# Kernel tuning notes

Hardware: AMD Instinct MI355X
Metric: run time of the kernel (lower is better)

Reference implementation:

```python
import jax, jax.numpy as jnp
import numpy as np

EPS = 1e-6
NUM_HEADS = 8
HEAD_DIM = 64
ROPE_BASE = 100.0


def _rope_cos_sin(dim, height, width, base=ROPE_BASE):
    quarter = dim // 4
    inv_freq = 1.0 / (base ** (jnp.arange(quarter, dtype=jnp.float32) / quarter))
    freqs_y = jnp.arange(height, dtype=jnp.float32)[:, None] * inv_freq  # (H, q)
    emb_y = jnp.concatenate([freqs_y, freqs_y], axis=-1)                 # (H, dim//2)
    freqs_x = jnp.arange(width, dtype=jnp.float32)[:, None] * inv_freq
    emb_x = jnp.concatenate([freqs_x, freqs_x], axis=-1)                 # (W, dim//2)
    emb_y_grid = jnp.broadcast_to(emb_y[:, None, :], (height, width, dim // 2))
    emb_x_grid = jnp.broadcast_to(emb_x[None, :, :], (height, width, dim // 2))
    full = jnp.concatenate([emb_y_grid, emb_x_grid], axis=-1).reshape(-1, dim)  # (H*W, dim)
    return jnp.cos(full), jnp.sin(full)


def _rotate_half(x):
    x1, x2 = jnp.split(x, 2, axis=-1)
    return jnp.concatenate([-x2, x1], axis=-1)


def setup_inputs() -> dict:
    key = jax.random.key(0)
    ks = jax.random.split(key, 8)
    B, C, H, W = 16, 512, 32, 32
    t_dim = 512
    inner = NUM_HEADS * HEAD_DIM  # 512
    s = 0.02
    return {
        "x": jax.random.normal(ks[0], (B, C, H, W), dtype=jnp.float32),
        "time_emb": jax.random.normal(ks[1], (B, t_dim), dtype=jnp.float32),
        "tm_w1": jax.random.normal(ks[2], (t_dim, t_dim), dtype=jnp.float32) * s,
        "tm_b1": jnp.zeros((t_dim,), dtype=jnp.float32),
        "tm_w2": jax.random.normal(ks[3], (t_dim, 2 * C), dtype=jnp.float32) * s,
        "tm_b2": jnp.zeros((2 * C,), dtype=jnp.float32),
        "qkv_w": jax.random.normal(ks[4], (C, 3 * inner), dtype=jnp.float32) * s,
        "out_w": jax.random.normal(ks[5], (inner, C), dtype=jnp.float32) * s,
        "out_b": jnp.zeros((C,), dtype=jnp.float32),
    }


def reference(x, time_emb, tm_w1, tm_b1, tm_w2, tm_b2, qkv_w, out_w, out_b):
    B, C, H, W = x.shape
    N = H * W
    h, d = NUM_HEADS, HEAD_DIM

    # AdaCLN: channel-wise layernorm with time-conditioned affine modulation
    u = jnp.mean(x, axis=1, keepdims=True)
    s = jnp.mean((x - u) ** 2, axis=1, keepdims=True)
    x_norm = (x - u) / jnp.sqrt(s + EPS)
    emb = jax.nn.silu(time_emb @ tm_w1 + tm_b1) @ tm_w2 + tm_b2  # (B, 2C)
    gamma, beta = jnp.split(emb, 2, axis=1)
    x_norm = x_norm * (1.0 + gamma[:, :, None, None]) + beta[:, :, None, None]

    # (B, C, H, W) -> (B, N, C)
    tokens = x_norm.transpose(0, 2, 3, 1).reshape(B, N, C)

    qkv = tokens @ qkv_w  # (B, N, 3*inner)
    q, k, v = jnp.split(qkv, 3, axis=-1)
    q = q.reshape(B, N, h, d).transpose(0, 2, 1, 3)  # (B, h, N, d)
    k = k.reshape(B, N, h, d).transpose(0, 2, 1, 3)
    v = v.reshape(B, N, h, d).transpose(0, 2, 1, 3)

    cos, sin = _rope_cos_sin(d, H, W)  # (N, d)
    q = q * cos + _rotate_half(q) * sin
    k = k * cos + _rotate_half(k) * sin

    # SDPA, scale = 1/sqrt(head_dim)
    scale = 1.0 / jnp.sqrt(jnp.asarray(d, dtype=q.dtype))
    scores = jnp.einsum("bhqd,bhkd->bhqk", q, k) * scale
    attn = jax.nn.softmax(scores, axis=-1)
    out = jnp.einsum("bhqk,bhkd->bhqd", attn, v)  # (B, h, N, d)

    out = out.transpose(0, 2, 1, 3).reshape(B, N, h * d)
    out = out @ out_w + out_b  # (B, N, C)
    out = out.reshape(B, H, W, C).transpose(0, 3, 1, 2)
    return x + out
```

## Files before the change

### kernel.cpp

```cpp
#include <hip/hip_runtime.h>
#include <stdint.h>
#include <stddef.h>

#define B_  16
#define C_  512
#define N_  1024
#define NH  8
#define HD  64

typedef __attribute__((ext_vector_type(8))) short bf16x8;
typedef __attribute__((ext_vector_type(4))) float f32x4;
typedef __attribute__((ext_vector_type(2))) __bf16 bf16x2t;
typedef __attribute__((ext_vector_type(2))) unsigned uint2v;

__device__ __forceinline__ float bf2f(short s) {
    unsigned u = ((unsigned)(unsigned short)s) << 16;
    return __builtin_bit_cast(float, u);
}
__device__ __forceinline__ unsigned packcvt(float lo, float hi) {
    bf16x2t v = { (__bf16)lo, (__bf16)hi };
    return __builtin_bit_cast(unsigned, v);
}
__device__ __forceinline__ short f2bf_hw(float f) {
    __bf16 b = (__bf16)f;
    return __builtin_bit_cast(short, b);
}
__device__ __forceinline__ float fexp2(float x) {
#if __has_builtin(__builtin_amdgcn_exp2f)
    return __builtin_amdgcn_exp2f(x);
#else
    return exp2f(x);
#endif
}
__device__ __forceinline__ void plswap32(unsigned& a, unsigned& b) {
#if __has_builtin(__builtin_amdgcn_permlane32_swap)
    uint2v r = __builtin_amdgcn_permlane32_swap(a, b, false, false);
    a = r.x; b = r.y;
#else
    unsigned ax = (unsigned)__shfl_xor((int)a, 32, 64), bx = (unsigned)__shfl_xor((int)b, 32, 64);
    bool hi = (threadIdx.x & 32) != 0;
    unsigned na = hi ? bx : a, nb = hi ? b : ax;
    a = na; b = nb;
#endif
}
__device__ __forceinline__ void plswap16(unsigned& a, unsigned& b) {
#if __has_builtin(__builtin_amdgcn_permlane16_swap)
    uint2v r = __builtin_amdgcn_permlane16_swap(a, b, false, false);
    a = r.x; b = r.y;
#else
    unsigned ax = (unsigned)__shfl_xor((int)a, 16, 64), bx = (unsigned)__shfl_xor((int)b, 16, 64);
    bool hi = (threadIdx.x & 16) != 0;
    unsigned na = hi ? bx : a, nb = hi ? b : ax;
    a = na; b = nb;
#endif
}
__device__ __forceinline__ float bcf(unsigned u) { return __builtin_bit_cast(float, u); }
__device__ __forceinline__ unsigned bcu(float f) { return __builtin_bit_cast(unsigned, f); }
__device__ __forceinline__ float redsum_lg(float x) {
    unsigned a = bcu(x), b = a; plswap32(a, b);
    float s = bcf(a) + bcf(b);
    a = bcu(s); b = a; plswap16(a, b);
    return bcf(a) + bcf(b);
}

#define MFMA16(a, b, c) __builtin_amdgcn_mfma_f32_16x16x32_bf16((a), (b), (c), 0, 0, 0)

typedef __attribute__((address_space(3))) unsigned int lds_u32;
typedef __attribute__((address_space(1))) unsigned int glb_u32;
__device__ __forceinline__ void gload16(const void* g, void* l) {
    __builtin_amdgcn_global_load_lds((const glb_u32*)g, (lds_u32*)l, 16, 0, 0);
}

__global__ __launch_bounds__(256) void k_prep(
        const float* __restrict__ qkv_w, const float* __restrict__ out_w,
        short* __restrict__ qkvwT, short* __restrict__ outwT,
        float4* __restrict__ ropetab) {
    int bid = blockIdx.x, tid = threadIdx.x;
    if (bid < 256) {
        const float* src; short* dst; int J, jt, kt;
        if (bid < 192) { src = qkv_w; dst = qkvwT; J = 1536; jt = (bid % 24) * 64; kt = (bid / 24) * 64; }
        else { int b2 = bid - 192; src = out_w; dst = outwT; J = 512; jt = (b2 & 7) * 64; kt = (b2 >> 3) * 64; }
        __shared__ float ts[64][65];
        int r = tid >> 4, c4 = (tid & 15) * 4;
        for (int rr = 0; rr < 64; rr += 16) {
            float4 v = *(const float4*)(src + (size_t)(kt + rr + r) * J + jt + c4);
            ts[c4 + 0][rr + r] = v.x;
            ts[c4 + 1][rr + r] = v.y;
            ts[c4 + 2][rr + r] = v.z;
            ts[c4 + 3][rr + r] = v.w;
        }
        __syncthreads();
        int jr = tid >> 2, kc = (tid & 3) * 16;
        unsigned w[8];
#pragma unroll
        for (int i = 0; i < 8; i++) w[i] = packcvt(ts[jr][kc + 2 * i], ts[jr][kc + 2 * i + 1]);
        short* dp = dst + (size_t)(jt + jr) * 512 + kt + kc;
        *(uint4*)(dp)     = make_uint4(w[0], w[1], w[2], w[3]);
        *(uint4*)(dp + 8) = make_uint4(w[4], w[5], w[6], w[7]);
    } else {
        int idx = (bid - 256) * 256 + tid;
        int n = idx >> 5, dq = idx & 31, i = dq & 15;
        float w = powf(100.0f, -(float)i * (1.0f / 16.0f));
        float y = (float)(n >> 5), xx = (float)(n & 31);
        ropetab[idx] = make_float4(cosf(y * w), sinf(y * w), cosf(xx * w), sinf(xx * w));
    }
}

__global__ __launch_bounds__(256) void k_mlp1(
        const float* __restrict__ temb, const float* __restrict__ w1, const float* __restrict__ b1,
        float* __restrict__ h) {
    int b = blockIdx.y, jt = blockIdx.x, tid = threadIdx.x;
    int jl = tid & 31, j = jt * 32 + jl, ks = tid >> 5;
    __shared__ float tl[512];
    __shared__ float ps[8][32];
    tl[tid] = temb[b * 512 + tid];
    tl[tid + 256] = temb[b * 512 + tid + 256];
    __syncthreads();
    float acc = 0.f;
    const float* wp = w1 + (size_t)(ks * 64) * 512 + j;
#pragma unroll 8
    for (int kk = 0; kk < 64; kk++) acc += tl[ks * 64 + kk] * wp[(size_t)kk * 512];
    ps[ks][jl] = acc;
    __syncthreads();
    if (tid < 32) {
        float s = ((ps[0][tid] + ps[1][tid]) + (ps[2][tid] + ps[3][tid]))
                + ((ps[4][tid] + ps[5][tid]) + (ps[6][tid] + ps[7][tid]));
        s += b1[jt * 32 + tid];
        h[b * 512 + jt * 32 + tid] = s / (1.0f + __expf(-s));
    }
}

__global__ __launch_bounds__(256) void k_mlp2(
        const float* __restrict__ h, const float* __restrict__ w2, const float* __restrict__ b2,
        float* __restrict__ gbout) {
    int b = blockIdx.y, jt = blockIdx.x, tid = threadIdx.x;
    int jl = tid & 31, j = jt * 32 + jl, ks = tid >> 5;
    __shared__ float hl[512];
    __shared__ float ps[8][32];
    hl[tid] = h[b * 512 + tid];
    hl[tid + 256] = h[b * 512 + tid + 256];
    __syncthreads();
    float acc = 0.f;
    const float* wp = w2 + (size_t)(ks * 64) * 1024 + j;
#pragma unroll 8
    for (int kk = 0; kk < 64; kk++) acc += hl[ks * 64 + kk] * wp[(size_t)kk * 1024];
    ps[ks][jl] = acc;
    __syncthreads();
    if (tid < 32) {
        float s = ((ps[0][tid] + ps[1][tid]) + (ps[2][tid] + ps[3][tid]))
                + ((ps[4][tid] + ps[5][tid]) + (ps[6][tid] + ps[7][tid]));
        gbout[b * 1024 + jt * 32 + tid] = s + b2[jt * 32 + tid];
    }
}

__global__ __launch_bounds__(256) void k_adacln(
        const float* __restrict__ x, const float* __restrict__ gb, short* __restrict__ tokens) {
    int b = blockIdx.y, n0 = blockIdx.x * 64;
    int tid = threadIdx.x, pix = tid & 63, sl = tid >> 6;
    const float* xb = x + (size_t)b * C_ * N_;
    __shared__ float rs[4][64], rq[4][64], mean_s[64], rstd_s[64];
    __shared__ float xs[64][65];

    float sum = 0.f, sq = 0.f;
    for (int ci = 0; ci < 128; ci++) {
        int c = sl * 128 + ci;
        float v = xb[(size_t)c * N_ + n0 + pix];
        sum += v; sq += v * v;
    }
    rs[sl][pix] = sum; rq[sl][pix] = sq;
    __syncthreads();
    if (tid < 64) {
        float s1 = rs[0][tid] + rs[1][tid] + rs[2][tid] + rs[3][tid];
        float s2 = rq[0][tid] + rq[1][tid] + rq[2][tid] + rq[3][tid];
        float mu = s1 * (1.0f / 512.0f);
        float var = s2 * (1.0f / 512.0f) - mu * mu;
        mean_s[tid] = mu;
        rstd_s[tid] = rsqrtf(var + 1e-6f);
    }
    const float* gam = gb + b * 1024;
    const float* bet = gam + 512;
    int ch = tid & 7;
    for (int ct = 0; ct < 8; ct++) {
        __syncthreads();
        for (int it = 0; it < 16; it++) {
            int cl = it * 4 + sl;
            xs[cl][pix] = xb[(size_t)(ct * 64 + cl) * N_ + n0 + pix];
        }
        __syncthreads();
#pragma unroll
        for (int pp = 0; pp < 2; pp++) {
            int p = pp * 32 + (tid >> 3);
            float mu = mean_s[p], rt = rstd_s[p];
            float v[8];
#pragma unroll
            for (int j = 0; j < 8; j++) {
                int c = ct * 64 + ch * 8 + j;
                v[j] = (xs[ch * 8 + j][p] - mu) * rt * (1.0f + gam[c]) + bet[c];
            }
            uint4 ov = make_uint4(packcvt(v[0], v[1]), packcvt(v[2], v[3]),
                                  packcvt(v[4], v[5]), packcvt(v[6], v[7]));
            *(uint4*)(tokens + ((size_t)(b * N_ + n0 + p)) * C_ + ct * 64 + ch * 8) = ov;
        }
    }
}

__global__ __launch_bounds__(256) void k_gemm_qkv(
        const short* __restrict__ A, const short* __restrict__ Bt,
        const float4* __restrict__ ropetab,
        short* __restrict__ qr, short* __restrict__ kr, short* __restrict__ vt) {
    __shared__ short Asm[128 * 32];
    __shared__ short Bsm[128 * 32];
    int wgid = blockIdx.x;
    int orig = (wgid & 7) * 192 + (wgid >> 3);
    int bx = orig % 12, by = orig / 12;
    int tid = threadIdx.x, wv = tid >> 6, ln = tid & 63;
    int wr = wv >> 1, wc = wv & 1, lr = ln & 15, lg = ln >> 4;
    const short* Ab = A + (size_t)by * 128 * 512;
    const short* Bb = Bt + (size_t)bx * 128 * 512;
    f32x4 acc[4][4] = {};
    int srow = ln >> 2, sch = ln & 3;
    for (int kb = 0; kb < 512; kb += 32) {
        int r0 = wv * 32;
        const short* ga = Ab + (size_t)(r0 + srow) * 512 + kb + sch * 8;
        gload16(ga, (void*)(Asm + r0 * 32));
        gload16(ga + 16 * 512, (void*)(Asm + (r0 + 16) * 32));
        const short* gbp = Bb + (size_t)(r0 + srow) * 512 + kb + sch * 8;
        gload16(gbp, (void*)(Bsm + r0 * 32));
        gload16(gbp + 16 * 512, (void*)(Bsm + (r0 + 16) * 32));
        __syncthreads();
        bf16x8 af[4], bfr[4];
#pragma unroll
        for (int m = 0; m < 4; m++) af[m] = *(const bf16x8*)(Asm + (wr * 64 + m * 16 + lr) * 32 + lg * 8);
#pragma unroll
        for (int f = 0; f < 4; f++) bfr[f] = *(const bf16x8*)(Bsm + (wc * 64 + f * 16 + lr) * 32 + lg * 8);
#pragma unroll
        for (int m = 0; m < 4; m++)
#pragma unroll
            for (int f = 0; f < 4; f++)
                acc[m][f] = MFMA16(af[m], bfr[f], acc[m][f]);
        __syncthreads();
    }
    int mbase = by * 128;
    int sec = bx >> 2;
    int h = (2 * bx + wc) & 7;
    if (sec < 2) {
        short* dst0 = (sec == 0) ? qr : kr;
#pragma unroll
        for (int m = 0; m < 4; m++) {
            int gmb = mbase + wr * 64 + m * 16 + lg * 4;
#pragma unroll
            for (int r = 0; r < 4; r++) {
                int gm = gmb + r; int b = gm >> 10, n = gm & 1023;
                short* rowp = dst0 + (((size_t)b * NH + h) * N_ + n) * HD;
                const float4* tr = ropetab + n * 32;
#pragma unroll
                for (int f2 = 0; f2 < 2; f2++) {
                    int d_lo = f2 * 16 + lr;
                    float4 t = tr[d_lo];
                    float a = acc[m][f2][r], bb2 = acc[m][f2 + 2][r];
                    rowp[d_lo]      = f2bf_hw(a * t.x - bb2 * t.y);
                    rowp[d_lo + 32] = f2bf_hw(bb2 * t.z + a * t.w);
                }
            }
        }
    } else {
#pragma unroll
        for (int m = 0; m < 4; m++) {
            int gmb = mbase + wr * 64 + m * 16 + lg * 4;
            int b = gmb >> 10, n0 = gmb & 1023;
#pragma unroll
            for (int f = 0; f < 4; f++) {
                int d = f * 16 + lr;
                uint2 val;
                val.x = packcvt(acc[m][f][0], acc[m][f][1]);
                val.y = packcvt(acc[m][f][2], acc[m][f][3]);
                *(uint2*)(vt + (((size_t)b * NH + h) * HD + d) * N_ + n0) = val;
            }
        }
    }
}

__global__ __launch_bounds__(512) void k_flash10(
        const short* __restrict__ qr, const short* __restrict__ kr, const short* __restrict__ vt,
        short* __restrict__ attn_out) {
    __shared__ short Ks[3][4096];
    __shared__ short Vs[3][4096];
    int bh = blockIdx.x, b = bh >> 3, h = bh & 7;
    int qt = blockIdx.y;
    int tid = threadIdx.x, wv = tid >> 6, ln = tid & 63;
    int lr = ln & 15, lg = ln >> 4;
    int qhalf = wv >> 2, w4 = wv & 3;
    const short* Qb = qr + ((size_t)bh * N_ + qt * 256 + qhalf * 128 + w4 * 32) * HD;
    const short* Kb = kr + (size_t)bh * N_ * HD;
    const short* Vb = vt + (size_t)bh * HD * N_;

    const float QSCALE = 0.125f * 1.44269504f;
    bf16x8 qf[2][2];
#pragma unroll
    for (int qg = 0; qg < 2; qg++)
#pragma unroll
        for (int hf = 0; hf < 2; hf++) {
            bf16x8 raw = *(const bf16x8*)(Qb + (qg * 16 + lr) * 64 + hf * 32 + lg * 8);
            bf16x8 sc;
#pragma unroll
            for (int j = 0; j < 8; j++) sc[j] = f2bf_hw(bf2f(raw[j]) * QSCALE);
            qf[qg][hf] = sc;
        }

    int srow = ln >> 3, cpos = ln & 7;
    int rloc = wv * 8 + srow;
    int csrc = cpos ^ (srow & 7);

    float l_part[2] = {0.f, 0.f};
    f32x4 ao[2][4] = {};

    asm volatile("s_waitcnt vmcnt(0)" ::: "memory");
    __builtin_amdgcn_sched_barrier(0);

#pragma unroll
    for (int t0 = 0; t0 < 2; t0++) {
        gload16(Kb + ((size_t)(t0 * 64 + rloc)) * 64 + csrc * 8,
                (void*)&Ks[t0][rloc * 64]);
        gload16(Vb + ((size_t)rloc) * 1024 + t0 * 64 + csrc * 8,
                (void*)&Vs[t0][rloc * 64]);
    }
    asm volatile("s_waitcnt vmcnt(2)" ::: "memory");
    __builtin_amdgcn_s_barrier();
    __builtin_amdgcn_sched_barrier(0);

    for (int kt = 0; kt < 16; kt++) {
        int cur = kt % 3;
        if (kt < 14) {
            int nxt = (kt + 2) % 3, ktn = kt + 2;
            gload16(Kb + ((size_t)(ktn * 64 + rloc)) * 64 + csrc * 8,
                    (void*)&Ks[nxt][rloc * 64]);
            gload16(Vb + ((size_t)rloc) * 1024 + ktn * 64 + csrc * 8,
                    (void*)&Vs[nxt][rloc * 64]);
        }

        f32x4 sT[2][4];
#pragma unroll
        for (int f = 0; f < 4; f++) {
            int r = f * 16 + lr;
            const short* kp = &Ks[cur][r * 64];
            bf16x8 ka  = *(const bf16x8*)(kp + ((lg ^ (r & 7)) * 8));
            bf16x8 kb2 = *(const bf16x8*)(kp + (((4 + lg) ^ (r & 7)) * 8));
#pragma unroll
            for (int qg = 0; qg < 2; qg++) {
                f32x4 s = {};
                s = MFMA16(ka, qf[qg][0], s);
                s = MFMA16(kb2, qf[qg][1], s);
                sT[qg][f] = s;
            }
        }

        union U4 { unsigned u[4]; bf16x8 v; };
        U4 pb[2][2];
#pragma unroll
        for (int qg = 0; qg < 2; qg++) {
            float rsum = 0.f;
            unsigned pk[4][2];
#pragma unroll
            for (int f = 0; f < 4; f++) {
                float p0 = fexp2(sT[qg][f][0]);
                float p1 = fexp2(sT[qg][f][1]);
                float p2 = fexp2(sT[qg][f][2]);
                float p3 = fexp2(sT[qg][f][3]);
                rsum += (p0 + p1) + (p2 + p3);
                pk[f][0] = packcvt(p0, p1);
                pk[f][1] = packcvt(p2, p3);
            }
            l_part[qg] += rsum;

#pragma unroll
            for (int kb = 0; kb < 2; kb++) {
                unsigned a = pk[2 * kb][0], c = pk[2 * kb + 1][0];
                plswap32(a, c); plswap16(a, c);
                pb[qg][kb].u[0] = a; pb[qg][kb].u[2] = c;
                unsigned bb = pk[2 * kb][1], d = pk[2 * kb + 1][1];
                plswap32(bb, d); plswap16(bb, d);
                pb[qg][kb].u[1] = bb; pb[qg][kb].u[3] = d;
            }
        }

#pragma unroll
        for (int dt = 0; dt < 4; dt++) {
            int rr = dt * 16 + lr;
            const short* vp = &Vs[cur][rr * 64];
            bf16x8 va0 = *(const bf16x8*)(vp + ((lg ^ (rr & 7)) * 8));
            bf16x8 va1 = *(const bf16x8*)(vp + (((4 + lg) ^ (rr & 7)) * 8));
#pragma unroll
            for (int qg = 0; qg < 2; qg++) {
                ao[qg][dt] = MFMA16(va0, pb[qg][0].v, ao[qg][dt]);
                ao[qg][dt] = MFMA16(va1, pb[qg][1].v, ao[qg][dt]);
            }
        }

        if (kt < 15) {
            if (kt < 14) asm volatile("s_waitcnt vmcnt(2)" ::: "memory");
            else         asm volatile("s_waitcnt vmcnt(0)" ::: "memory");
            __builtin_amdgcn_s_barrier();
            __builtin_amdgcn_sched_barrier(0);
        }
    }

#pragma unroll
    for (int qg = 0; qg < 2; qg++) {
        float inv = 1.0f / redsum_lg(l_part[qg]);
        int qglob = qt * 256 + qhalf * 128 + w4 * 32 + qg * 16 + lr;
        size_t ob = ((size_t)b * N_ + qglob) * 512 + h * 64 + lg * 4;
#pragma unroll
        for (int dt = 0; dt < 4; dt++) {
            uint2 val;
            val.x = packcvt(ao[qg][dt][0] * inv, ao[qg][dt][1] * inv);
            val.y = packcvt(ao[qg][dt][2] * inv, ao[qg][dt][3] * inv);
            *(uint2*)(attn_out + ob + dt * 16) = val;
        }
    }
}

__global__ __launch_bounds__(256) void k_gemm_out(
        const short* __restrict__ A, const short* __restrict__ Bt,
        const float* __restrict__ x, const float* __restrict__ obias, float* __restrict__ out) {
    __shared__ short Asm[128 * 32];
    __shared__ short Bsm[128 * 32];
    int tid = threadIdx.x, wv = tid >> 6, ln = tid & 63;
    int wr = wv >> 1, wc = wv & 1, lr = ln & 15, lg = ln >> 4;
    const short* Ab = A + (size_t)blockIdx.y * 128 * 512;
    const short* Bb = Bt + (size_t)blockIdx.x * 128 * 512;
    f32x4 acc[4][4] = {};
    int srow = ln >> 2, sch = ln & 3;
    for (int kb = 0; kb < 512; kb += 32) {
        int r0 = wv * 32;
        const short* ga = Ab + (size_t)(r0 + srow) * 512 + kb + sch * 8;
        gload16(ga, (void*)(Asm + r0 * 32));
        gload16(ga + 16 * 512, (void*)(Asm + (r0 + 16) * 32));
        const short* gbp = Bb + (size_t)(r0 + srow) * 512 + kb + sch * 8;
        gload16(gbp, (void*)(Bsm + r0 * 32));
        gload16(gbp + 16 * 512, (void*)(Bsm + (r0 + 16) * 32));
        __syncthreads();
        bf16x8 af[4], bfr[4];
#pragma unroll
        for (int m = 0; m < 4; m++) af[m] = *(const bf16x8*)(Asm + (wr * 64 + m * 16 + lr) * 32 + lg * 8);
#pragma unroll
        for (int f = 0; f < 4; f++) bfr[f] = *(const bf16x8*)(Bsm + (wc * 64 + f * 16 + lr) * 32 + lg * 8);
#pragma unroll
        for (int m = 0; m < 4; m++)
#pragma unroll
            for (int f = 0; f < 4; f++)
                acc[m][f] = MFMA16(af[m], bfr[f], acc[m][f]);
        __syncthreads();
    }
    int cb = blockIdx.y * 128 + wr * 64, tb = blockIdx.x * 128 + wc * 64;
#pragma unroll
    for (int m = 0; m < 4; m++) {
#pragma unroll
        for (int f = 0; f < 4; f++) {
            int gt = tb + f * 16 + lr;
            int b = gt >> 10, n = gt & 1023;
#pragma unroll
            for (int r = 0; r < 4; r++) {
                int gc = cb + m * 16 + lg * 4 + r;
                size_t ad = ((size_t)b * C_ + gc) * N_ + n;
                out[ad] = acc[m][f][r] + obias[gc] + x[ad];
            }
        }
    }
}

extern "C" void kernel_launch(void* const* d_in, const int* in_sizes, int n_in,
                              void* d_out, int out_size, void* d_ws, size_t ws_size,
                              hipStream_t stream) {
    const float* x     = (const float*)d_in[0];
    const float* temb  = (const float*)d_in[1];
    const float* tm_w1 = (const float*)d_in[2];
    const float* tm_b1 = (const float*)d_in[3];
    const float* tm_w2 = (const float*)d_in[4];
    const float* tm_b2 = (const float*)d_in[5];
    const float* qkv_w = (const float*)d_in[6];
    const float* out_w = (const float*)d_in[7];
    const float* out_b = (const float*)d_in[8];
    float* out = (float*)d_out;

    char* ws = (char*)d_ws;
    short*  qkvwT  = (short*)(ws);
    short*  outwT  = (short*)(ws + 1572864);
    float4* ropetab= (float4*)(ws + 2097152);
    float*  gb     = (float*)(ws + 2621440);
    short*  tokens = (short*)(ws + 2686976);
    short*  qr     = (short*)(ws + 19464192);
    short*  kr     = (short*)(ws + 36241408);
    short*  vt     = (short*)(ws + 53018624);
    short*  attn   = tokens;
    float*  hbuf   = (float*)(ws + 2686976);

    k_prep<<<dim3(384), dim3(256), 0, stream>>>(qkv_w, out_w, qkvwT, outwT, ropetab);
    k_mlp1<<<dim3(16, 16), dim3(256), 0, stream>>>(temb, tm_w1, tm_b1, hbuf);
    k_mlp2<<<dim3(32, 16), dim3(256), 0, stream>>>(hbuf, tm_w2, tm_b2, gb);
    k_adacln<<<dim3(16, 16), dim3(256), 0, stream>>>(x, gb, tokens);
    k_gemm_qkv<<<dim3(1536), dim3(256), 0, stream>>>(tokens, qkvwT, ropetab, qr, kr, vt);
    k_flash10<<<dim3(128, 4), dim3(512), 0, stream>>>(qr, kr, vt, attn);
    k_gemm_out<<<dim3(128, 4), dim3(256), 0, stream>>>(outwT, attn, x, out_b, out);
}
```

Measured before the change: 147.8 us.

## Triple-buffer LDS tiles in QKV and output GEMMs with async prefetch

Both the QKV and output-projection GEMMs move from a single shared-memory tile with two barriers per k-step to a three-stage ring buffer. Global-to-LDS loads run two k-tiles ahead, and there is one barrier per step with explicit vmcnt waits, so memory latency overlaps the MFMA work. LDS use per block triples to 48KB, which may lower occupancy. Correctness depends on the hand-written waitcnt counts matching the number of outstanding loads.

Measured after the change: 151.7 us. +2.7%, slower.

```diff
diff --git a/kernel.cpp b/kernel.cpp
--- a/kernel.cpp
+++ b/kernel.cpp
@@ -208,8 +208,8 @@
         const short* __restrict__ A, const short* __restrict__ Bt,
         const float4* __restrict__ ropetab,
         short* __restrict__ qr, short* __restrict__ kr, short* __restrict__ vt) {
-    __shared__ short Asm[128 * 32];
-    __shared__ short Bsm[128 * 32];
+    __shared__ short Asm[3][4096];
+    __shared__ short Bsm[3][4096];
     int wgid = blockIdx.x;
     int orig = (wgid & 7) * 192 + (wgid >> 3);
     int bx = orig % 12, by = orig / 12;
@@ -219,26 +219,48 @@
     const short* Bb = Bt + (size_t)bx * 128 * 512;
     f32x4 acc[4][4] = {};
     int srow = ln >> 2, sch = ln & 3;
-    for (int kb = 0; kb < 512; kb += 32) {
-        int r0 = wv * 32;
-        const short* ga = Ab + (size_t)(r0 + srow) * 512 + kb + sch * 8;
-        gload16(ga, (void*)(Asm + r0 * 32));
-        gload16(ga + 16 * 512, (void*)(Asm + (r0 + 16) * 32));
-        const short* gbp = Bb + (size_t)(r0 + srow) * 512 + kb + sch * 8;
-        gload16(gbp, (void*)(Bsm + r0 * 32));
-        gload16(gbp + 16 * 512, (void*)(Bsm + (r0 + 16) * 32));
-        __syncthreads();
+    int r0 = wv * 32;
+
+#pragma unroll
+    for (int t0 = 0; t0 < 2; t0++) {
+        const short* ga = Ab + (size_t)(r0 + srow) * 512 + t0 * 32 + sch * 8;
+        gload16(ga, (void*)(&Asm[t0][r0 * 32]));
+        gload16(ga + 16 * 512, (void*)(&Asm[t0][(r0 + 16) * 32]));
+        const short* gbp = Bb + (size_t)(r0 + srow) * 512 + t0 * 32 + sch * 8;
+        gload16(gbp, (void*)(&Bsm[t0][r0 * 32]));
+        gload16(gbp + 16 * 512, (void*)(&Bsm[t0][(r0 + 16) * 32]));
+    }
+    asm volatile("s_waitcnt vmcnt(4)" ::: "memory");
+    __builtin_amdgcn_s_barrier();
+    __builtin_amdgcn_sched_barrier(0);
+
+    for (int kt = 0; kt < 16; kt++) {
+        int cur = kt % 3;
+        if (kt < 14) {
+            int nxt = (kt + 2) % 3, kb = (kt + 2) * 32;
+            const short* ga = Ab + (size_t)(r0 + srow) * 512 + kb + sch * 8;
+            gload16(ga, (void*)(&Asm[nxt][r0 * 32]));
+            gload16(ga + 16 * 512, (void*)(&Asm[nxt][(r0 + 16) * 32]));
+            const short* gbp = Bb + (size_t)(r0 + srow) * 512 + kb + sch * 8;
+            gload16(gbp, (void*)(&Bsm[nxt][r0 * 32]));
+            gload16(gbp + 16 * 512, (void*)(&Bsm[nxt][(r0 + 16) * 32]));
+        }
         bf16x8 af[4], bfr[4];
 #pragma unroll
-        for (int m = 0; m < 4; m++) af[m] = *(const bf16x8*)(Asm + (wr * 64 + m * 16 + lr) * 32 + lg * 8);
-#pragma unroll
-        for (int f = 0; f < 4; f++) bfr[f] = *(const bf16x8*)(Bsm + (wc * 64 + f * 16 + lr) * 32 + lg * 8);
+        for (int m = 0; m < 4; m++) af[m] = *(const bf16x8*)(&Asm[cur][(wr * 64 + m * 16 + lr) * 32 + lg * 8]);
+#pragma unroll
+        for (int f = 0; f < 4; f++) bfr[f] = *(const bf16x8*)(&Bsm[cur][(wc * 64 + f * 16 + lr) * 32 + lg * 8]);
 #pragma unroll
         for (int m = 0; m < 4; m++)
 #pragma unroll
             for (int f = 0; f < 4; f++)
                 acc[m][f] = MFMA16(af[m], bfr[f], acc[m][f]);
-        __syncthreads();
+        if (kt < 15) {
+            if (kt < 14) asm volatile("s_waitcnt vmcnt(4)" ::: "memory");
+            else         asm volatile("s_waitcnt vmcnt(0)" ::: "memory");
+            __builtin_amdgcn_s_barrier();
+            __builtin_amdgcn_sched_barrier(0);
+        }
     }
     int mbase = by * 128;
     int sec = bx >> 2;
@@ -422,34 +444,56 @@
 __global__ __launch_bounds__(256) void k_gemm_out(
         const short* __restrict__ A, const short* __restrict__ Bt,
         const float* __restrict__ x, const float* __restrict__ obias, float* __restrict__ out) {
-    __shared__ short Asm[128 * 32];
-    __shared__ short Bsm[128 * 32];
+    __shared__ short Asm[3][4096];
+    __shared__ short Bsm[3][4096];
     int tid = threadIdx.x, wv = tid >> 6, ln = tid & 63;
     int wr = wv >> 1, wc = wv & 1, lr = ln & 15, lg = ln >> 4;
     const short* Ab = A + (size_t)blockIdx.y * 128 * 512;
     const short* Bb = Bt + (size_t)blockIdx.x * 128 * 512;
     f32x4 acc[4][4] = {};
     int srow = ln >> 2, sch = ln & 3;
-    for (int kb = 0; kb < 512; kb += 32) {
-        int r0 = wv * 32;
-        const short* ga = Ab + (size_t)(r0 + srow) * 512 + kb + sch * 8;
-        gload16(ga, (void*)(Asm + r0 * 32));
-        gload16(ga + 16 * 512, (void*)(Asm + (r0 + 16) * 32));
-        const short* gbp = Bb + (size_t)(r0 + srow) * 512 + kb + sch * 8;
-        gload16(gbp, (void*)(Bsm + r0 * 32));
-        gload16(gbp + 16 * 512, (void*)(Bsm + (r0 + 16) * 32));
-        __syncthreads();
+    int r0 = wv * 32;
+
+#pragma unroll
+    for (int t0 = 0; t0 < 2; t0++) {
+        const short* ga = Ab + (size_t)(r0 + srow) * 512 + t0 * 32 + sch * 8;
+        gload16(ga, (void*)(&Asm[t0][r0 * 32]));
+        gload16(ga + 16 * 512, (void*)(&Asm[t0][(r0 + 16) * 32]));
+        const short* gbp = Bb + (size_t)(r0 + srow) * 512 + t0 * 32 + sch * 8;
+        gload16(gbp, (void*)(&Bsm[t0][r0 * 32]));
+        gload16(gbp + 16 * 512, (void*)(&Bsm[t0][(r0 + 16) * 32]));
+    }
+    asm volatile("s_waitcnt vmcnt(4)" ::: "memory");
+    __builtin_amdgcn_s_barrier();
+    __builtin_amdgcn_sched_barrier(0);
+
+    for (int kt = 0; kt < 16; kt++) {
+        int cur = kt % 3;
+        if (kt < 14) {
+            int nxt = (kt + 2) % 3, kb = (kt + 2) * 32;
+            const short* ga = Ab + (size_t)(r0 + srow) * 512 + kb + sch * 8;
+            gload16(ga, (void*)(&Asm[nxt][r0 * 32]));
+            gload16(ga + 16 * 512, (void*)(&Asm[nxt][(r0 + 16) * 32]));
+            const short* gbp = Bb + (size_t)(r0 + srow) * 512 + kb + sch * 8;
+            gload16(gbp, (void*)(&Bsm[nxt][r0 * 32]));
+            gload16(gbp + 16 * 512, (void*)(&Bsm[nxt][(r0 + 16) * 32]));
+        }
         bf16x8 af[4], bfr[4];
 #pragma unroll
-        for (int m = 0; m < 4; m++) af[m] = *(const bf16x8*)(Asm + (wr * 64 + m * 16 + lr) * 32 + lg * 8);
-#pragma unroll
-        for (int f = 0; f < 4; f++) bfr[f] = *(const bf16x8*)(Bsm + (wc * 64 + f * 16 + lr) * 32 + lg * 8);
+        for (int m = 0; m < 4; m++) af[m] = *(const bf16x8*)(&Asm[cur][(wr * 64 + m * 16 + lr) * 32 + lg * 8]);
+#pragma unroll
+        for (int f = 0; f < 4; f++) bfr[f] = *(const bf16x8*)(&Bsm[cur][(wc * 64 + f * 16 + lr) * 32 + lg * 8]);
 #pragma unroll
         for (int m = 0; m < 4; m++)
 #pragma unroll
             for (int f = 0; f < 4; f++)
                 acc[m][f] = MFMA16(af[m], bfr[f], acc[m][f]);
-        __syncthreads();
+        if (kt < 15) {
+            if (kt < 14) asm volatile("s_waitcnt vmcnt(4)" ::: "memory");
+            else         asm volatile("s_waitcnt vmcnt(0)" ::: "memory");
+            __builtin_amdgcn_s_barrier();
+            __builtin_amdgcn_sched_barrier(0);
+        }
     }
     int cb = blockIdx.y * 128 + wr * 64, tb = blockIdx.x * 128 + wc * 64;
 #pragma unroll
```
